# Kernel tuning notes

Measured on AMD Instinct MI355X. Metric: run time of the kernel, lower is better.

## Reference

```python
import jax, jax.numpy as jnp
import numpy as np

HID = 256
POS_FREQ = 10
DIR_FREQ = 4
POS_ENC = 3 * (2 * POS_FREQ + 1)   # 63
DIR_ENC = 3 * (2 * DIR_FREQ + 1)   # 27
N_PTS = 262144


def _posenc(x, num_freq):
    freqs = (2.0 ** jnp.arange(num_freq)).astype(x.dtype)      # [F]
    xf = x[..., None, :] * freqs[:, None]                       # [..., F, D]
    sc = jnp.stack([jnp.sin(xf), jnp.cos(xf)], axis=-2)         # [..., F, 2, D]
    return jnp.concatenate([x, sc.reshape(*x.shape[:-1], -1)], axis=-1)


def _linear_init(key, fan_in, fan_out):
    kw, kb = jax.random.split(key)
    s = 1.0 / np.sqrt(fan_in)
    W = jax.random.uniform(kw, (fan_in, fan_out), jnp.float32, -s, s)
    b = jax.random.uniform(kb, (fan_out,), jnp.float32, -s, s)
    return W, b


def setup_inputs() -> dict:
    key = jax.random.key(0)
    ks = jax.random.split(key, 16)
    inp = {
        "positions": jax.random.normal(ks[0], (N_PTS, 3), jnp.float32),
        "directions": jax.random.normal(ks[1], (N_PTS, 3), jnp.float32),
    }
    W, b = _linear_init(ks[2], POS_ENC, HID)
    inp["W_in"], inp["b_in"] = W, b
    # 7 hidden layers; layer index 4 takes skip concat (HID + POS_ENC)
    for i in range(7):
        fan_in = HID + POS_ENC if i == 4 else HID
        W, b = _linear_init(ks[3 + i], fan_in, HID)
        inp[f"W_h{i}"], inp[f"b_h{i}"] = W, b
    W, b = _linear_init(ks[10], HID, HID + 1)
    inp["W_out"], inp["b_out"] = W, b
    W, b = _linear_init(ks[11], HID + DIR_ENC, HID // 2)
    inp["W_r1"], inp["b_r1"] = W, b
    W, b = _linear_init(ks[12], HID // 2, 3)
    inp["W_r2"], inp["b_r2"] = W, b
    return inp


def _forward(positions, directions, W_in, b_in, hidden_params, W_out, b_out,
             W_r1, b_r1, W_r2, b_r2):
    pe = _posenc(positions, POS_FREQ)    # [N, 63]
    de = _posenc(directions, DIR_FREQ)   # [N, 27]
    h = jax.nn.relu(pe @ W_in + b_in)    # [N, 256]
    for i, (W, b) in enumerate(hidden_params):
        if i == 4:
            h = jnp.concatenate([h, pe], axis=-1)  # skip connection [N, 319]
        h = jax.nn.relu(h @ W + b)
    out = h @ W_out + b_out                      # [N, 257]
    features = out[..., :HID]                    # [N, 256]
    density = jax.nn.relu(out[..., HID:HID + 1])  # [N, 1]
    rgb_in = jnp.concatenate([features, de], axis=-1)  # [N, 283]
    rgb = jax.nn.sigmoid(jax.nn.relu(rgb_in @ W_r1 + b_r1) @ W_r2 + b_r2)  # [N, 3]
    return rgb, density


def reference(positions, directions, W_in, b_in,
              W_h0, b_h0, W_h1, b_h1, W_h2, b_h2, W_h3, b_h3,
              W_h4, b_h4, W_h5, b_h5, W_h6, b_h6,
              W_out, b_out, W_r1, b_r1, W_r2, b_r2):
    hidden = [(W_h0, b_h0), (W_h1, b_h1), (W_h2, b_h2), (W_h3, b_h3),
              (W_h4, b_h4), (W_h5, b_h5), (W_h6, b_h6)]
    return _forward(positions, directions, W_in, b_in, hidden,
                    W_out, b_out, W_r1, b_r1, W_r2, b_r2)
```

## Files before the change

kernel.cpp:

```cpp
#include <hip/hip_runtime.h>
#include <math.h>

#define NPTS 262144
#define MT 64

typedef __attribute__((ext_vector_type(8))) short bf16x8;
typedef __attribute__((ext_vector_type(4))) float f32x4;
typedef __attribute__((ext_vector_type(2))) unsigned int u32x2;

#if defined(__has_builtin)
#if __has_builtin(__builtin_amdgcn_cvt_pk_bf16_f32)
#define HAVE_CVT_PK_BF16 1
#endif
#endif

__device__ __forceinline__ short f2bf(float f) {
    union { float f; unsigned u; } v; v.f = f;
    unsigned r = v.u + 0x7fffu + ((v.u >> 16) & 1u);
    return (short)(r >> 16);
}
__device__ __forceinline__ unsigned pk2(float a, float b) {
#ifdef HAVE_CVT_PK_BF16
    auto r = __builtin_amdgcn_cvt_pk_bf16_f32(a, b);
    unsigned u; __builtin_memcpy(&u, &r, 4);
    return u;
#else
    return ((unsigned)(unsigned short)f2bf(a)) |
           ((unsigned)(unsigned short)f2bf(b) << 16);
#endif
}

#define OFF_IN   0
#define SZ_IN    (64*256)
#define OFF_H0   (OFF_IN + SZ_IN)
#define SZ_H     (256*256)
#define OFF_H1   (OFF_H0 + SZ_H)
#define OFF_H2   (OFF_H1 + SZ_H)
#define OFF_H3   (OFF_H2 + SZ_H)
#define OFF_H4   (OFF_H3 + SZ_H)
#define SZ_H4    (320*256)
#define OFF_H5   (OFF_H4 + SZ_H4)
#define OFF_H6   (OFF_H5 + SZ_H)
#define OFF_OUT  (OFF_H6 + SZ_H)
#define SZ_OUT   (256*272)
#define OFF_R1   (OFF_OUT + SZ_OUT)
#define SZ_R1    (288*128)
#define OFF_R2   (OFF_R1 + SZ_R1)
#define SZ_R2    (128*16)
#define WS_TOTAL (OFF_R2 + SZ_R2)

struct PrepP { const float* W[11]; short* ws; };

__global__ __launch_bounds__(256) void prep_all(PrepP pp) {
    int i = blockIdx.x * 256 + threadIdx.x;
    if (i >= WS_TOTAL) return;
    const int offs[12] = {OFF_IN, OFF_H0, OFF_H1, OFF_H2, OFF_H3, OFF_H4,
                          OFF_H5, OFF_H6, OFF_OUT, OFF_R1, OFF_R2, WS_TOTAL};
    const int Ks[11]  = {63,256,256,256,256,319,256,256,256,283,128};
    const int Ns[11]  = {256,256,256,256,256,256,256,256,257,128,3};
    const int Nps[11] = {256,256,256,256,256,256,256,256,272,128,16};
    int seg = 0;
    while (i >= offs[seg + 1]) seg++;
    int li = i - offs[seg];
    int j = li & 7, L = (li >> 3) & 63, tile = li >> 9;
    int nNt = Nps[seg] >> 4;
    int nt = tile % nNt, kt = tile / nNt;
    int k = kt * 32 + ((L >> 4) << 3) + j;
    int n = nt * 16 + (L & 15);
    float v = (k < Ks[seg] && n < Ns[seg]) ? pp.W[seg][k * Ns[seg] + n] : 0.f;
    pp.ws[i] = f2bf(v);
}

struct Params {
    const float *pos, *dir;
    const float *b_in, *b_h0, *b_h1, *b_h2, *b_h3, *b_h4, *b_h5, *b_h6;
    const float *b_out, *b_r1, *b_r2;
    const short *w;
    float *out;
};

template<int NKT, int NT, int NS, int MODE>
__device__ __forceinline__ void layerT(const short* __restrict__ Wsw,
                                       const float* __restrict__ bias,
                                       short* X, float* dout, int p0,
                                       int ntB, int wave, int lane) {
    const int l15 = lane & 15, quad = lane >> 4;
    __syncthreads();
    const short* xb = X + quad * 512 + l15 * 8;

    if (MODE == 1 && wave < 4) {
        f32x4 ad = (f32x4){0.f, 0.f, 0.f, 0.f};
#pragma unroll
        for (int kt = 0; kt < NKT; ++kt) {
            bf16x8 b = *(const bf16x8*)(xb + wave * 128 + kt * 2048);
            bf16x8 a = *(const bf16x8*)(Wsw + (size_t)((kt * NT + 16) * 64 + lane) * 8);
            ad = __builtin_amdgcn_mfma_f32_16x16x32_bf16(a, b, ad, 0, 0, 0);
        }
        if (quad == 0)
            dout[3 * NPTS + p0 + wave * 16 + l15] = fmaxf(ad[0] + bias[256], 0.f);
    }

    f32x4 acc[NS][4];
#pragma unroll
    for (int s = 0; s < NS; s++)
#pragma unroll
        for (int t = 0; t < 4; t++) acc[s][t] = (f32x4){0.f, 0.f, 0.f, 0.f};

    const short* wp = Wsw + (size_t)(ntB * 64 + lane) * 8;

    bf16x8 a_c[NS], b_c[4];
#pragma unroll
    for (int s = 0; s < NS; s++)
        a_c[s] = *(const bf16x8*)(wp + (size_t)s * 512);
#pragma unroll
    for (int t = 0; t < 4; t++)
        b_c[t] = *(const bf16x8*)(xb + t * 128);

#pragma unroll
    for (int kt = 0; kt < NKT; ++kt) {
        bf16x8 a_n[NS], b_n[4];
        if (kt + 1 < NKT) {
            const short* wp1 = wp + (size_t)(kt + 1) * NT * 512;
#pragma unroll
            for (int s = 0; s < NS; s++)
                a_n[s] = *(const bf16x8*)(wp1 + (size_t)s * 512);
#pragma unroll
            for (int t = 0; t < 4; t++)
                b_n[t] = *(const bf16x8*)(xb + (kt + 1) * 2048 + t * 128);
        }
#pragma unroll
        for (int s = 0; s < NS; s++)
#pragma unroll
            for (int t = 0; t < 4; t++)
                acc[s][t] = __builtin_amdgcn_mfma_f32_16x16x32_bf16(a_c[s], b_c[t], acc[s][t], 0, 0, 0);
        if (kt + 1 < NKT) {
#pragma unroll
            for (int s = 0; s < NS; s++) a_c[s] = a_n[s];
#pragma unroll
            for (int t = 0; t < 4; t++) b_c[t] = b_n[t];
        }
    }
    __syncthreads();
#pragma unroll
    for (int s = 0; s < NS; s++) {
        const int n0 = (ntB + s) * 16 + quad * 4;
        const f32x4 bv = *(const f32x4*)(bias + n0);
        short* xo = X + (2 * (ntB + s) + (quad >> 1)) * 512 + (quad & 1) * 4;
#pragma unroll
        for (int t = 0; t < 4; t++) {
            const int m = t * 16 + l15;
            float v0 = acc[s][t][0] + bv[0];
            float v1 = acc[s][t][1] + bv[1];
            float v2 = acc[s][t][2] + bv[2];
            float v3 = acc[s][t][3] + bv[3];
            if (MODE == 0) {
                v0 = fmaxf(v0, 0.f); v1 = fmaxf(v1, 0.f);
                v2 = fmaxf(v2, 0.f); v3 = fmaxf(v3, 0.f);
            }
            u32x2 w; w[0] = pk2(v0, v1); w[1] = pk2(v2, v3);
            *(u32x2*)(xo + m * 8) = w;
        }
    }
}

__global__ __launch_bounds__(512, 4) void nerf_fused(Params P) {
    __shared__ __align__(16) short X[40 * 512];
    const int tid = threadIdx.x;
    const int wave = tid >> 6, lane = tid & 63;
    const int p0 = blockIdx.x * MT;

    const int ntB_h = wave * 2;

    for (int i = tid; i < MT * 64; i += 512) {
        const int pt = i & 63, d = i >> 6;
        float v = 0.f;
        if (d < 3) v = P.pos[(p0 + pt) * 3 + d];
        else if (d < 63) {
            const int e = d - 3, f = e / 6, r = e % 6;
            const float x = P.pos[(p0 + pt) * 3 + (r % 3)];
            const float xf = x * (float)(1 << f);
            v = (r < 3) ? sinf(xf) : cosf(xf);
        }
        const short bv = f2bf(v);
        X[((d >> 3) * 64 + pt) * 8 + (d & 7)] = bv;
        X[((32 + (d >> 3)) * 64 + pt) * 8 + (d & 7)] = bv;
    }

    layerT<2, 16, 2, 0>(P.w + OFF_IN, P.b_in, X, P.out, p0, ntB_h, wave, lane);
    layerT<8, 16, 2, 0>(P.w + OFF_H0, P.b_h0, X, P.out, p0, ntB_h, wave, lane);
    layerT<8, 16, 2, 0>(P.w + OFF_H1, P.b_h1, X, P.out, p0, ntB_h, wave, lane);
    layerT<8, 16, 2, 0>(P.w + OFF_H2, P.b_h2, X, P.out, p0, ntB_h, wave, lane);
    layerT<8, 16, 2, 0>(P.w + OFF_H3, P.b_h3, X, P.out, p0, ntB_h, wave, lane);
    layerT<10, 16, 2, 0>(P.w + OFF_H4, P.b_h4, X, P.out, p0, ntB_h, wave, lane);
    layerT<8, 16, 2, 0>(P.w + OFF_H5, P.b_h5, X, P.out, p0, ntB_h, wave, lane);
    layerT<8, 16, 2, 0>(P.w + OFF_H6, P.b_h6, X, P.out, p0, ntB_h, wave, lane);
    layerT<8, 17, 2, 1>(P.w + OFF_OUT, P.b_out, X, P.out, p0, ntB_h, wave, lane);

    for (int i = tid; i < MT * 32; i += 512) {
        const int pt = i & 63, d = i >> 6;
        float v = 0.f;
        if (d < 3) v = P.dir[(p0 + pt) * 3 + d];
        else if (d < 27) {
            const int e = d - 3, f = e / 6, r = e % 6;
            const float x = P.dir[(p0 + pt) * 3 + (r % 3)];
            const float xf = x * (float)(1 << f);
            v = (r < 3) ? sinf(xf) : cosf(xf);
        }
        X[((32 + (d >> 3)) * 64 + pt) * 8 + (d & 7)] = f2bf(v);
    }

    layerT<9, 8, 1, 0>(P.w + OFF_R1, P.b_r1, X, P.out, p0, wave, wave, lane);

    __syncthreads();
    if (wave < 4) {
        const int l15 = lane & 15, quad = lane >> 4;
        f32x4 acc = (f32x4){0.f, 0.f, 0.f, 0.f};
        const short* xb = X + quad * 512 + (wave * 16 + l15) * 8;
#pragma unroll
        for (int kt = 0; kt < 4; ++kt) {
            bf16x8 b = *(const bf16x8*)(xb + kt * 2048);
            bf16x8 a = *(const bf16x8*)(P.w + OFF_R2 + (size_t)(kt * 64 + lane) * 8);
            acc = __builtin_amdgcn_mfma_f32_16x16x32_bf16(a, b, acc, 0, 0, 0);
        }
        if (quad == 0) {
#pragma unroll
            for (int r = 0; r < 3; r++) {
                const float v = acc[r] + P.b_r2[r];
                P.out[(size_t)(p0 + wave * 16 + l15) * 3 + r] = 1.f / (1.f + expf(-v));
            }
        }
    }
}

extern "C" void kernel_launch(void* const* d_in, const int* in_sizes, int n_in,
                              void* d_out, int out_size, void* d_ws, size_t ws_size,
                              hipStream_t stream) {
    short* ws = (short*)d_ws;

    PrepP pp;
    pp.W[0]  = (const float*)d_in[2];
    pp.W[1]  = (const float*)d_in[4];
    pp.W[2]  = (const float*)d_in[6];
    pp.W[3]  = (const float*)d_in[8];
    pp.W[4]  = (const float*)d_in[10];
    pp.W[5]  = (const float*)d_in[12];
    pp.W[6]  = (const float*)d_in[14];
    pp.W[7]  = (const float*)d_in[16];
    pp.W[8]  = (const float*)d_in[18];
    pp.W[9]  = (const float*)d_in[20];
    pp.W[10] = (const float*)d_in[22];
    pp.ws = ws;
    hipLaunchKernelGGL(prep_all, dim3((WS_TOTAL + 255) / 256), dim3(256), 0, stream, pp);

    Params P;
    P.pos  = (const float*)d_in[0];
    P.dir  = (const float*)d_in[1];
    P.b_in = (const float*)d_in[3];
    P.b_h0 = (const float*)d_in[5];
    P.b_h1 = (const float*)d_in[7];
    P.b_h2 = (const float*)d_in[9];
    P.b_h3 = (const float*)d_in[11];
    P.b_h4 = (const float*)d_in[13];
    P.b_h5 = (const float*)d_in[15];
    P.b_h6 = (const float*)d_in[17];
    P.b_out = (const float*)d_in[19];
    P.b_r1 = (const float*)d_in[21];
    P.b_r2 = (const float*)d_in[23];
    P.w = ws;
    P.out = (float*)d_out;
    hipLaunchKernelGGL(nerf_fused, dim3(NPTS / MT), dim3(512), 0, stream, P);
}
```

Measured before the change: 412.1 us.

## Ping-pong activation buffers, prefetch weights two k-steps ahead, vectorize encoding

Activations now alternate between two shared-memory buffers across layers, so each layer needs only one barrier instead of two. Weight fragments are prefetched two k-tiles ahead, and the first ones are loaded before the barrier. Positional and directional encodings are computed per thread and written to shared memory as one 16-byte store. The direction encoding is kept in registers and inserted later. The cost is a larger LDS footprint (about 72KB per block instead of 40KB), which can lower the number of resident blocks per CU and add register pressure.

```diff
diff --git a/kernel.cpp b/kernel.cpp
--- a/kernel.cpp
+++ b/kernel.cpp
@@ -82,11 +82,23 @@
 template<int NKT, int NT, int NS, int MODE>
 __device__ __forceinline__ void layerT(const short* __restrict__ Wsw,
                                        const float* __restrict__ bias,
-                                       short* X, float* dout, int p0,
+                                       const short* Xin, short* Xout,
+                                       float* dout, int p0,
                                        int ntB, int wave, int lane) {
     const int l15 = lane & 15, quad = lane >> 4;
+    const short* xb = Xin + quad * 512 + l15 * 8;
+    const short* wp = Wsw + (size_t)(ntB * 64 + lane) * 8;
+
+    bf16x8 a0[NS], a1[NS];
+#pragma unroll
+    for (int s = 0; s < NS; s++)
+        a0[s] = *(const bf16x8*)(wp + (size_t)s * 512);
+    if (NKT > 1)
+#pragma unroll
+        for (int s = 0; s < NS; s++)
+            a1[s] = *(const bf16x8*)(wp + (size_t)NT * 512 + s * 512);
+
     __syncthreads();
-    const short* xb = X + quad * 512 + l15 * 8;
 
     if (MODE == 1 && wave < 4) {
         f32x4 ad = (f32x4){0.f, 0.f, 0.f, 0.f};
@@ -106,46 +118,57 @@
 #pragma unroll
         for (int t = 0; t < 4; t++) acc[s][t] = (f32x4){0.f, 0.f, 0.f, 0.f};
 
-    const short* wp = Wsw + (size_t)(ntB * 64 + lane) * 8;
-
-    bf16x8 a_c[NS], b_c[4];
-#pragma unroll
-    for (int s = 0; s < NS; s++)
-        a_c[s] = *(const bf16x8*)(wp + (size_t)s * 512);
+    bf16x8 b_c[4];
 #pragma unroll
     for (int t = 0; t < 4; t++)
         b_c[t] = *(const bf16x8*)(xb + t * 128);
 
 #pragma unroll
     for (int kt = 0; kt < NKT; ++kt) {
-        bf16x8 a_n[NS], b_n[4];
+        bf16x8 b_n[4], a_n[NS];
         if (kt + 1 < NKT) {
-            const short* wp1 = wp + (size_t)(kt + 1) * NT * 512;
-#pragma unroll
-            for (int s = 0; s < NS; s++)
-                a_n[s] = *(const bf16x8*)(wp1 + (size_t)s * 512);
 #pragma unroll
             for (int t = 0; t < 4; t++)
                 b_n[t] = *(const bf16x8*)(xb + (kt + 1) * 2048 + t * 128);
         }
-#pragma unroll
-        for (int s = 0; s < NS; s++)
-#pragma unroll
-            for (int t = 0; t < 4; t++)
-                acc[s][t] = __builtin_amdgcn_mfma_f32_16x16x32_bf16(a_c[s], b_c[t], acc[s][t], 0, 0, 0);
+        if (kt + 2 < NKT) {
+#pragma unroll
+            for (int s = 0; s < NS; s++)
+                a_n[s] = *(const bf16x8*)(wp + (size_t)(kt + 2) * NT * 512 + s * 512);
+        }
+        if ((kt & 1) == 0) {
+#pragma unroll
+            for (int s = 0; s < NS; s++)
+#pragma unroll
+                for (int t = 0; t < 4; t++)
+                    acc[s][t] = __builtin_amdgcn_mfma_f32_16x16x32_bf16(a0[s], b_c[t], acc[s][t], 0, 0, 0);
+        } else {
+#pragma unroll
+            for (int s = 0; s < NS; s++)
+#pragma unroll
+                for (int t = 0; t < 4; t++)
+                    acc[s][t] = __builtin_amdgcn_mfma_f32_16x16x32_bf16(a1[s], b_c[t], acc[s][t], 0, 0, 0);
+        }
+        if (kt + 2 < NKT) {
+            if ((kt & 1) == 0) {
+#pragma unroll
+                for (int s = 0; s < NS; s++) a0[s] = a_n[s];
+            } else {
+#pragma unroll
+                for (int s = 0; s < NS; s++) a1[s] = a_n[s];
+            }
+        }
         if (kt + 1 < NKT) {
 #pragma unroll
-            for (int s = 0; s < NS; s++) a_c[s] = a_n[s];
-#pragma unroll
             for (int t = 0; t < 4; t++) b_c[t] = b_n[t];
         }
     }
-    __syncthreads();
+
 #pragma unroll
     for (int s = 0; s < NS; s++) {
         const int n0 = (ntB + s) * 16 + quad * 4;
         const f32x4 bv = *(const f32x4*)(bias + n0);
-        short* xo = X + (2 * (ntB + s) + (quad >> 1)) * 512 + (quad & 1) * 4;
+        short* xo = Xout + (2 * (ntB + s) + (quad >> 1)) * 512 + (quad & 1) * 4;
 #pragma unroll
         for (int t = 0; t < 4; t++) {
             const int m = t * 16 + l15;
@@ -164,58 +187,79 @@
 }
 
 __global__ __launch_bounds__(512, 4) void nerf_fused(Params P) {
-    __shared__ __align__(16) short X[40 * 512];
+    __shared__ __align__(16) short XA[32 * 512];
+    __shared__ __align__(16) short XB[40 * 512];
     const int tid = threadIdx.x;
     const int wave = tid >> 6, lane = tid & 63;
     const int p0 = blockIdx.x * MT;
 
     const int ntB_h = wave * 2;
 
-    for (int i = tid; i < MT * 64; i += 512) {
-        const int pt = i & 63, d = i >> 6;
-        float v = 0.f;
-        if (d < 3) v = P.pos[(p0 + pt) * 3 + d];
-        else if (d < 63) {
-            const int e = d - 3, f = e / 6, r = e % 6;
-            const float x = P.pos[(p0 + pt) * 3 + (r % 3)];
-            const float xf = x * (float)(1 << f);
-            v = (r < 3) ? sinf(xf) : cosf(xf);
-        }
-        const short bv = f2bf(v);
-        X[((d >> 3) * 64 + pt) * 8 + (d & 7)] = bv;
-        X[((32 + (d >> 3)) * 64 + pt) * 8 + (d & 7)] = bv;
-    }
-
-    layerT<2, 16, 2, 0>(P.w + OFF_IN, P.b_in, X, P.out, p0, ntB_h, wave, lane);
-    layerT<8, 16, 2, 0>(P.w + OFF_H0, P.b_h0, X, P.out, p0, ntB_h, wave, lane);
-    layerT<8, 16, 2, 0>(P.w + OFF_H1, P.b_h1, X, P.out, p0, ntB_h, wave, lane);
-    layerT<8, 16, 2, 0>(P.w + OFF_H2, P.b_h2, X, P.out, p0, ntB_h, wave, lane);
-    layerT<8, 16, 2, 0>(P.w + OFF_H3, P.b_h3, X, P.out, p0, ntB_h, wave, lane);
-    layerT<10, 16, 2, 0>(P.w + OFF_H4, P.b_h4, X, P.out, p0, ntB_h, wave, lane);
-    layerT<8, 16, 2, 0>(P.w + OFF_H5, P.b_h5, X, P.out, p0, ntB_h, wave, lane);
-    layerT<8, 16, 2, 0>(P.w + OFF_H6, P.b_h6, X, P.out, p0, ntB_h, wave, lane);
-    layerT<8, 17, 2, 1>(P.w + OFF_OUT, P.b_out, X, P.out, p0, ntB_h, wave, lane);
-
-    for (int i = tid; i < MT * 32; i += 512) {
-        const int pt = i & 63, d = i >> 6;
-        float v = 0.f;
-        if (d < 3) v = P.dir[(p0 + pt) * 3 + d];
-        else if (d < 27) {
-            const int e = d - 3, f = e / 6, r = e % 6;
-            const float x = P.dir[(p0 + pt) * 3 + (r % 3)];
-            const float xf = x * (float)(1 << f);
-            v = (r < 3) ? sinf(xf) : cosf(xf);
-        }
-        X[((32 + (d >> 3)) * 64 + pt) * 8 + (d & 7)] = f2bf(v);
-    }
-
-    layerT<9, 8, 1, 0>(P.w + OFF_R1, P.b_r1, X, P.out, p0, wave, wave, lane);
+    {
+        const int pt = tid & 63, g = tid >> 6;
+        const float x0 = P.pos[(p0 + pt) * 3 + 0];
+        const float x1 = P.pos[(p0 + pt) * 3 + 1];
+        const float x2 = P.pos[(p0 + pt) * 3 + 2];
+        bf16x8 v;
+#pragma unroll
+        for (int j = 0; j < 8; j++) {
+            const int d = g * 8 + j;
+            float val = 0.f;
+            if (d < 3) val = (d == 0) ? x0 : (d == 1) ? x1 : x2;
+            else if (d < 63) {
+                const int e = d - 3, f = e / 6, r = e % 6;
+                const float x = (r % 3 == 0) ? x0 : (r % 3 == 1) ? x1 : x2;
+                const float xf = x * (float)(1 << f);
+                val = (r < 3) ? sinf(xf) : cosf(xf);
+            }
+            v[j] = f2bf(val);
+        }
+        *(bf16x8*)(XA + ((size_t)g * 64 + pt) * 8) = v;
+        *(bf16x8*)(XB + ((size_t)(32 + g) * 64 + pt) * 8) = v;
+    }
+
+    bf16x8 de_v;
+    if (wave < 4) {
+        const int pt = tid & 63, g = wave;
+        const float x0 = P.dir[(p0 + pt) * 3 + 0];
+        const float x1 = P.dir[(p0 + pt) * 3 + 1];
+        const float x2 = P.dir[(p0 + pt) * 3 + 2];
+#pragma unroll
+        for (int j = 0; j < 8; j++) {
+            const int d = g * 8 + j;
+            float val = 0.f;
+            if (d < 3) val = (d == 0) ? x0 : (d == 1) ? x1 : x2;
+            else if (d < 27) {
+                const int e = d - 3, f = e / 6, r = e % 6;
+                const float x = (r % 3 == 0) ? x0 : (r % 3 == 1) ? x1 : x2;
+                const float xf = x * (float)(1 << f);
+                val = (r < 3) ? sinf(xf) : cosf(xf);
+            }
+            de_v[j] = f2bf(val);
+        }
+    }
+
+    layerT<2, 16, 2, 0>(P.w + OFF_IN, P.b_in, XA, XB, P.out, p0, ntB_h, wave, lane);
+    layerT<8, 16, 2, 0>(P.w + OFF_H0, P.b_h0, XB, XA, P.out, p0, ntB_h, wave, lane);
+    layerT<8, 16, 2, 0>(P.w + OFF_H1, P.b_h1, XA, XB, P.out, p0, ntB_h, wave, lane);
+    layerT<8, 16, 2, 0>(P.w + OFF_H2, P.b_h2, XB, XA, P.out, p0, ntB_h, wave, lane);
+    layerT<8, 16, 2, 0>(P.w + OFF_H3, P.b_h3, XA, XB, P.out, p0, ntB_h, wave, lane);
+    layerT<10, 16, 2, 0>(P.w + OFF_H4, P.b_h4, XB, XA, P.out, p0, ntB_h, wave, lane);
+    layerT<8, 16, 2, 0>(P.w + OFF_H5, P.b_h5, XA, XB, P.out, p0, ntB_h, wave, lane);
+
+    if (wave < 4)
+        *(bf16x8*)(XB + ((size_t)(32 + wave) * 64 + (tid & 63)) * 8) = de_v;
+
+    layerT<8, 16, 2, 0>(P.w + OFF_H6, P.b_h6, XB, XA, P.out, p0, ntB_h, wave, lane);
+    layerT<8, 17, 2, 1>(P.w + OFF_OUT, P.b_out, XA, XB, P.out, p0, ntB_h, wave, lane);
+
+    layerT<9, 8, 1, 0>(P.w + OFF_R1, P.b_r1, XB, XA, P.out, p0, wave, wave, lane);
 
     __syncthreads();
     if (wave < 4) {
         const int l15 = lane & 15, quad = lane >> 4;
         f32x4 acc = (f32x4){0.f, 0.f, 0.f, 0.f};
-        const short* xb = X + quad * 512 + (wave * 16 + l15) * 8;
+        const short* xb = XA + quad * 512 + (wave * 16 + l15) * 8;
 #pragma unroll
         for (int kt = 0; kt < 4; ++kt) {
             bf16x8 b = *(const bf16x8*)(xb + kt * 2048);
```

New measurement: 409.4 us. Within noise of the previous version (-0.6%).
